# Performance work log

Measured on AMD Instinct MI355X. Metric: run time of the kernel, lower is better.

Reference implementation:

```python
import jax, jax.numpy as jnp
import numpy as np

N = 25000
E = 400000
RAW = 64
REP = 64
HID = 128
HEADS = 2
OUT = 2
NEG_SLOPE = 0.2


def setup_inputs() -> dict:
    key = jax.random.key(0)
    ks = jax.random.split(key, 16)
    d_in1 = RAW + REP
    d_h = HID * HEADS
    inp = {
        'x': jax.random.normal(ks[0], (N, RAW), jnp.float32),
        'rep': jax.random.normal(ks[1], (N, REP), jnp.float32),
        'src': jax.random.randint(ks[2], (E,), 0, N, jnp.int32),
        'dst': jax.random.randint(ks[3], (E,), 0, N, jnp.int32),
        # GATConv 1 params
        'W1': jax.random.normal(ks[4], (d_in1, d_h), jnp.float32) * (1.0 / np.sqrt(d_in1)),
        'al1': jax.random.normal(ks[5], (HEADS, HID), jnp.float32) * 0.1,
        'ar1': jax.random.normal(ks[6], (HEADS, HID), jnp.float32) * 0.1,
        'b1': jnp.zeros((HEADS, HID), jnp.float32),
        # GATConv 2 params
        'W2': jax.random.normal(ks[7], (d_h, d_h), jnp.float32) * (1.0 / np.sqrt(d_h)),
        'al2': jax.random.normal(ks[8], (HEADS, HID), jnp.float32) * 0.1,
        'ar2': jax.random.normal(ks[9], (HEADS, HID), jnp.float32) * 0.1,
        'b2': jnp.zeros((HEADS, HID), jnp.float32),
        # final edge classifier
        'fcW': jax.random.normal(ks[10], (d_h * 2, OUT), jnp.float32) * (1.0 / np.sqrt(d_h * 2)),
        'fcb': jnp.zeros((OUT,), jnp.float32),
    }
    return inp


def _gat_conv(feat, W, a_l, a_r, bias, src, dst):
    """DGL-style GATConv: proj -> edge LeakyReLU score -> per-dst softmax -> scatter-sum."""
    n = feat.shape[0]
    h = (feat @ W).reshape(n, HEADS, HID)            # [N,H,D]
    el = jnp.einsum('nhd,hd->nh', h, a_l)            # [N,H]
    er = jnp.einsum('nhd,hd->nh', h, a_r)            # [N,H]
    e = jax.nn.leaky_relu(el[src] + er[dst], NEG_SLOPE)  # [E,H]
    # numerically stable segment softmax over incoming edges of each dst node
    m = jax.ops.segment_max(e, dst, num_segments=n)      # [N,H]
    m = jnp.where(jnp.isfinite(m), m, 0.0)
    ex = jnp.exp(e - m[dst])                             # [E,H]
    s = jax.ops.segment_sum(ex, dst, num_segments=n)     # [N,H]
    alpha = ex / s[dst]                                  # [E,H]
    out = jax.ops.segment_sum(alpha[:, :, None] * h[src], dst, num_segments=n)  # [N,H,D]
    return out + bias[None, :, :]


def reference(x, rep, src, dst, W1, al1, ar1, b1, W2, al2, ar2, b2, fcW, fcb):
    feat = jnp.concatenate([x, rep], axis=-1)                       # [N, RAW+REP]
    h = _gat_conv(feat, W1, al1, ar1, b1, src, dst)                 # [N,H,D]
    h = jax.nn.relu(h.reshape(N, HEADS * HID))                      # [N, H*D]
    h = _gat_conv(h, W2, al2, ar2, b2, src, dst)                    # [N,H,D]
    h = jax.nn.relu(h.reshape(N, HEADS * HID))                      # [N, H*D]
    edge_feat = jnp.concatenate([h[src], h[dst]], axis=1)           # [E, 2*H*D]
    return edge_feat @ fcW + fcb                                    # [E, OUT]
```

## Files before the change

kernel.cpp:

```cpp
#include <hip/hip_runtime.h>
#include <hip/hip_bf16.h>

#define HEADS 2
#define HIDD  128
#define DH    256
#define NEG   0.2f
#define CAP   128

typedef _Float16 half4 __attribute__((ext_vector_type(4)));
typedef float    f32x4 __attribute__((ext_vector_type(4)));


__global__ __launch_bounds__(256) void k_prep(const float* __restrict__ x,
                                              const float* __restrict__ rep,
                                              const float* __restrict__ W1,
                                              const float* __restrict__ W2,
                                              const int* __restrict__ dst,
                                              _Float16* __restrict__ feat16,
                                              _Float16* __restrict__ W1T,
                                              _Float16* __restrict__ W2T,
                                              int* __restrict__ deg,
                                              int N, int E) {
    int gid = blockIdx.x * 256 + threadIdx.x;
    int featQuads = N * 32;
    if (gid < featQuads) {
        int n = gid >> 5, d = (gid & 31) * 4;
        const float* s = (d < 64) ? (x + (size_t)n * 64 + d) : (rep + (size_t)n * 64 + (d - 64));
        float4 v = *reinterpret_cast<const float4*>(s);
        half4 o = { (_Float16)v.x, (_Float16)v.y, (_Float16)v.z, (_Float16)v.w };
        *reinterpret_cast<half4*>(feat16 + (size_t)n * 128 + d) = o;
        return;
    }
    gid -= featQuads;
    if (gid < 256 * 128) {
        int n = gid >> 7, k = gid & 127;
        W1T[n * 128 + k] = (_Float16)W1[(size_t)k * 256 + n];
        return;
    }
    gid -= 256 * 128;
    if (gid < 256 * 256) {
        int n = gid >> 8, k = gid & 255;
        W2T[n * 256 + k] = (_Float16)W2[(size_t)k * 256 + n];
        return;
    }
    gid -= 256 * 256;
    if (gid < E) atomicAdd(&deg[dst[gid]], 1);
}


__global__ __launch_bounds__(1024) void k_scan(const int* __restrict__ deg,
                                               int* __restrict__ row_ptr,
                                               int* __restrict__ cursor, int n) {
    __shared__ int lds[1024];
    int tid = threadIdx.x;
    int base = tid * 32;
    int v[32];
#pragma unroll
    for (int k = 0; k < 8; ++k) {
        int4 q = *reinterpret_cast<const int4*>(deg + base + k * 4);
        v[k * 4 + 0] = q.x; v[k * 4 + 1] = q.y; v[k * 4 + 2] = q.z; v[k * 4 + 3] = q.w;
    }
    int local[32];
    int sum = 0;
#pragma unroll
    for (int k = 0; k < 32; ++k) { local[k] = sum; sum += v[k]; }
    lds[tid] = sum;
    __syncthreads();
    for (int off = 1; off < 1024; off <<= 1) {
        int t = (tid >= off) ? lds[tid - off] : 0;
        __syncthreads();
        lds[tid] += t;
        __syncthreads();
    }
    int thread_off = lds[tid] - sum;
#pragma unroll
    for (int k = 0; k < 32; ++k) {
        int i = base + k;
        if (i < n) {
            int rp = thread_off + local[k];
            row_ptr[i] = rp;
            cursor[i]  = rp;
        }
    }
    if (tid == 1023) row_ptr[n] = lds[1023];
}

__global__ void k_fill(const int* __restrict__ src, const int* __restrict__ dst,
                       int* __restrict__ cursor, int* __restrict__ csr_src, int E) {
    int e = blockIdx.x * blockDim.x + threadIdx.x;
    if (e < E) {
        int pos = atomicAdd(&cursor[dst[e]], 1);
        csr_src[pos] = src[e];
    }
}


#define GBM 64
#define GBN 128
#define GBK 64

template<int K>
__global__ __launch_bounds__(256) void k_gemm16(const _Float16* __restrict__ A,
                                                const _Float16* __restrict__ BT,
                                                _Float16* __restrict__ C16,
                                                const float* __restrict__ alp,
                                                const float* __restrict__ arp,
                                                float* __restrict__ el,
                                                float* __restrict__ er, int M) {
    __shared__ _Float16 As[2][GBM * GBK];
    __shared__ _Float16 Bs[2][GBN * GBK];

    int tid = threadIdx.x;
    int lane = tid & 63;
    int wave = tid >> 6;
    int row0 = blockIdx.x * GBM;
    int col0 = blockIdx.y * GBN;
    int wrow = (wave & 1) * 32;
    int wcol = (wave >> 1) * 64;

    uint4 ra[2], rb[4];
    const int am = tid >> 3;
    const int ak8 = (tid & 7) * 8;

    auto stage_load = [&](int s) {
        const _Float16* ap = A + (size_t)(row0 + am) * K + s * GBK + ak8;
        ra[0] = *reinterpret_cast<const uint4*>(ap);
        ra[1] = *reinterpret_cast<const uint4*>(ap + (size_t)32 * K);
        const _Float16* bp = BT + (size_t)(col0 + am) * K + s * GBK + ak8;
#pragma unroll
        for (int it = 0; it < 4; ++it)
            rb[it] = *reinterpret_cast<const uint4*>(bp + (size_t)(it * 32) * K);
    };
    auto stage_write = [&](int buf) {
        char* ab = (char*)As[buf];
        char* bb = (char*)Bs[buf];
#pragma unroll
        for (int it = 0; it < 2; ++it) {
            int m = am + it * 32;
            int byte = (m * 128 + ak8 * 2) ^ ((m & 7) << 4);
            *reinterpret_cast<uint4*>(ab + byte) = ra[it];
        }
#pragma unroll
        for (int it = 0; it < 4; ++it) {
            int n = am + it * 32;
            int byte = (n * 128 + ak8 * 2) ^ ((n & 7) << 4);
            *reinterpret_cast<uint4*>(bb + byte) = rb[it];
        }
    };

    f32x4 acc[2][4];
#pragma unroll
    for (int i = 0; i < 2; ++i)
#pragma unroll
        for (int j = 0; j < 4; ++j) acc[i][j] = (f32x4){0.f, 0.f, 0.f, 0.f};

    stage_load(0);
    stage_write(0);
    __syncthreads();

    const int S = K / GBK;
    for (int s = 0; s < S; ++s) {
        if (s + 1 < S) stage_load(s + 1);
        const char* ab = (const char*)As[s & 1];
        const char* bb = (const char*)Bs[s & 1];
#pragma unroll
        for (int kk = 0; kk < GBK / 16; ++kk) {
            half4 af[2], bf[4];
#pragma unroll
            for (int i = 0; i < 2; ++i) {
                int m = wrow + i * 16 + (lane & 15);
                int byte = (m * 128 + kk * 32 + (lane >> 4) * 8) ^ ((m & 7) << 4);
                af[i] = *reinterpret_cast<const half4*>(ab + byte);
            }
#pragma unroll
            for (int j = 0; j < 4; ++j) {
                int n = wcol + j * 16 + (lane & 15);
                int byte = (n * 128 + kk * 32 + (lane >> 4) * 8) ^ ((n & 7) << 4);
                bf[j] = *reinterpret_cast<const half4*>(bb + byte);
            }
#pragma unroll
            for (int i = 0; i < 2; ++i)
#pragma unroll
                for (int j = 0; j < 4; ++j)
                    acc[i][j] = __builtin_amdgcn_mfma_f32_16x16x16f16(af[i], bf[j], acc[i][j], 0, 0, 0);
        }
        if (s + 1 < S) stage_write((s + 1) & 1);
        __syncthreads();
    }

    char* Cs = (char*)As;
    {
        int r4 = (lane >> 4) * 4, cl = lane & 15;
#pragma unroll
        for (int i = 0; i < 2; ++i)
#pragma unroll
            for (int j = 0; j < 4; ++j) {
                int col = wcol + j * 16 + cl;
#pragma unroll
                for (int r = 0; r < 4; ++r) {
                    int row = wrow + i * 16 + r4 + r;
                    int byte = (row * 256 + col * 2) ^ ((row & 7) << 4);
                    *reinterpret_cast<_Float16*>(Cs + byte) = (_Float16)acc[i][j][r];
                }
            }
    }
    __syncthreads();

#pragma unroll
    for (int it = 0; it < 4; ++it) {
        int lin = tid + it * 256;
        int row = lin >> 4, chunk = lin & 15;
        int gr = row0 + row;
        if (gr < M) {
            int byte = (row * 256 + chunk * 16) ^ ((row & 7) << 4);
            *reinterpret_cast<uint4*>(C16 + (size_t)gr * DH + col0 + chunk * 8) =
                *reinterpret_cast<const uint4*>(Cs + byte);
        }
    }

    {
        int r = lane >> 2, q = lane & 3;
        int row = wave * 16 + r;
        const float* alg = alp + col0;
        const float* arg = arp + col0;
        float els = 0.f, ers = 0.f;
#pragma unroll
        for (int kk = 0; kk < 4; ++kk) {
            int c0 = q * 32 + kk * 8;
            int byte = (row * 256 + c0 * 2) ^ ((row & 7) << 4);
            uint4 u = *reinterpret_cast<const uint4*>(Cs + byte);
            const _Float16* hv = (const _Float16*)&u;
#pragma unroll
            for (int t = 0; t < 8; ++t) {
                float hvv = (float)hv[t];
                els = fmaf(hvv, alg[c0 + t], els);
                ers = fmaf(hvv, arg[c0 + t], ers);
            }
        }
        els += __shfl_xor(els, 1); els += __shfl_xor(els, 2);
        ers += __shfl_xor(ers, 1); ers += __shfl_xor(ers, 2);
        int gr = row0 + row;
        if (q == 0 && gr < M) {
            el[gr * 2 + blockIdx.y] = els;
            er[gr * 2 + blockIdx.y] = ers;
        }
    }
}


template<bool FINAL>
__global__ __launch_bounds__(256) void k_agg(const _Float16* __restrict__ h,
                                             const float2* __restrict__ el2,
                                             const float2* __restrict__ er2,
                                             const int* __restrict__ row_ptr,
                                             const int* __restrict__ csr_src,
                                             const float* __restrict__ bias,
                                             _Float16* __restrict__ g,
                                             const float* __restrict__ fcW,
                                             float* __restrict__ p, int N) {
    __shared__ int    s_idx[4][CAP];
    __shared__ float2 s_a[4][CAP];

    int w = threadIdx.x >> 6, lane = threadIdx.x & 63;
    int node = blockIdx.x * 4 + w;
    if (node >= N) return;
    int beg = row_ptr[node];
    int deg = row_ptr[node + 1] - beg;
    float2 er = er2[node];
    bool lo = lane < 32;

    float m0 = -__builtin_inff(), m1 = -__builtin_inff();
    for (int i = lane; i < deg; i += 64) {
        int s = csr_src[beg + i];
        float2 el = el2[s];
        float sc0 = el.x + er.x; sc0 = sc0 > 0.f ? sc0 : NEG * sc0;
        float sc1 = el.y + er.y; sc1 = sc1 > 0.f ? sc1 : NEG * sc1;
        if (i < CAP) { s_idx[w][i] = s; s_a[w][i] = make_float2(sc0, sc1); }
        m0 = fmaxf(m0, sc0);
        m1 = fmaxf(m1, sc1);
    }
#pragma unroll
    for (int off = 32; off; off >>= 1) {
        m0 = fmaxf(m0, __shfl_xor(m0, off));
        m1 = fmaxf(m1, __shfl_xor(m1, off));
    }

    float sum0 = 0.f, sum1 = 0.f;
    for (int i = lane; i < deg; i += 64) {
        float2 sc;
        if (i < CAP) sc = s_a[w][i];
        else {
            int s = csr_src[beg + i];
            float2 el = el2[s];
            sc.x = el.x + er.x; sc.x = sc.x > 0.f ? sc.x : NEG * sc.x;
            sc.y = el.y + er.y; sc.y = sc.y > 0.f ? sc.y : NEG * sc.y;
        }
        float e0 = __expf(sc.x - m0);
        float e1 = __expf(sc.y - m1);
        if (i < CAP) s_a[w][i] = make_float2(e0, e1);
        sum0 += e0;
        sum1 += e1;
    }
#pragma unroll
    for (int off = 32; off; off >>= 1) {
        sum0 += __shfl_xor(sum0, off);
        sum1 += __shfl_xor(sum1, off);
    }
    float S   = lo ? sum0 : sum1;
    float inv = S > 0.f ? 1.f / S : 0.f;
    float mh  = lo ? m0 : m1;
    float erh = lo ? er.x : er.y;

    const _Float16* hp = h + lane * 4;
    float4 acc = make_float4(0.f, 0.f, 0.f, 0.f);

#define FETCH(I, S_, A_)                                                    \
    do {                                                                     \
        int _i = (I);                                                        \
        if (_i < CAP) {                                                      \
            S_ = s_idx[w][_i];                                               \
            float2 _a2 = s_a[w][_i];                                         \
            A_ = lo ? _a2.x : _a2.y;                                         \
        } else {                                                             \
            S_ = csr_src[beg + _i];                                          \
            float2 _el = el2[S_];                                            \
            float _sc = (lo ? _el.x : _el.y) + erh;                          \
            _sc = _sc > 0.f ? _sc : NEG * _sc;                               \
            A_ = __expf(_sc - mh);                                           \
        }                                                                    \
    } while (0)

#define ACCUM(V, A_)                                                         \
    do {                                                                     \
        const _Float16* _hv = reinterpret_cast<const _Float16*>(&(V));       \
        acc.x = fmaf(A_, (float)_hv[0], acc.x);                              \
        acc.y = fmaf(A_, (float)_hv[1], acc.y);                              \
        acc.z = fmaf(A_, (float)_hv[2], acc.z);                              \
        acc.w = fmaf(A_, (float)_hv[3], acc.w);                              \
    } while (0)

    int i = 0;
    for (; i + 8 <= deg; i += 8) {
        int ss[8];
        float aa[8];
#pragma unroll
        for (int u = 0; u < 8; ++u) FETCH(i + u, ss[u], aa[u]);
        uint2 vv[8];
#pragma unroll
        for (int u = 0; u < 8; ++u)
            vv[u] = *reinterpret_cast<const uint2*>(hp + (size_t)ss[u] * DH);
#pragma unroll
        for (int u = 0; u < 8; ++u) ACCUM(vv[u], aa[u]);
    }
    for (; i + 4 <= deg; i += 4) {
        int ss[4];
        float aa[4];
#pragma unroll
        for (int u = 0; u < 4; ++u) FETCH(i + u, ss[u], aa[u]);
        uint2 vv[4];
#pragma unroll
        for (int u = 0; u < 4; ++u)
            vv[u] = *reinterpret_cast<const uint2*>(hp + (size_t)ss[u] * DH);
#pragma unroll
        for (int u = 0; u < 4; ++u) ACCUM(vv[u], aa[u]);
    }
    for (; i < deg; ++i) {
        int s;
        float a;
        FETCH(i, s, a);
        uint2 v = *reinterpret_cast<const uint2*>(hp + (size_t)s * DH);
        ACCUM(v, a);
    }
#undef FETCH
#undef ACCUM

    float4 b = *reinterpret_cast<const float4*>(bias + lane * 4);
    float o0 = fmaxf(fmaf(acc.x, inv, b.x), 0.f);
    float o1 = fmaxf(fmaf(acc.y, inv, b.y), 0.f);
    float o2 = fmaxf(fmaf(acc.z, inv, b.z), 0.f);
    float o3 = fmaxf(fmaf(acc.w, inv, b.w), 0.f);

    if (!FINAL) {
        half4 o = { (_Float16)o0, (_Float16)o1, (_Float16)o2, (_Float16)o3 };
        *reinterpret_cast<half4*>(g + (size_t)node * DH + lane * 4) = o;
    } else {
        int d = lane * 4;
        float a0 = 0.f, a1 = 0.f, a2 = 0.f, a3 = 0.f;
        float ov[4] = {o0, o1, o2, o3};
#pragma unroll
        for (int t = 0; t < 4; ++t) {
            float2 wt = *reinterpret_cast<const float2*>(&fcW[(d + t) * 2]);
            float2 wb = *reinterpret_cast<const float2*>(&fcW[(DH + d + t) * 2]);
            a0 = fmaf(ov[t], wt.x, a0);
            a1 = fmaf(ov[t], wt.y, a1);
            a2 = fmaf(ov[t], wb.x, a2);
            a3 = fmaf(ov[t], wb.y, a3);
        }
#pragma unroll
        for (int off = 32; off; off >>= 1) {
            a0 += __shfl_xor(a0, off);
            a1 += __shfl_xor(a1, off);
            a2 += __shfl_xor(a2, off);
            a3 += __shfl_xor(a3, off);
        }
        if (lane == 0)
            *reinterpret_cast<float4*>(&p[(size_t)node * 4]) = make_float4(a0, a1, a2, a3);
    }
}


__global__ void k_edgeout(const float* __restrict__ p,
                          const int* __restrict__ src,
                          const int* __restrict__ dst,
                          const float* __restrict__ fcb,
                          float* __restrict__ out, int E) {
    int e = blockIdx.x * blockDim.x + threadIdx.x;
    if (e >= E) return;
    int s = src[e], d = dst[e];
    float2 ps = *reinterpret_cast<const float2*>(&p[(size_t)s * 4]);
    float2 pd = *reinterpret_cast<const float2*>(&p[(size_t)d * 4 + 2]);
    float2 o;
    o.x = ps.x + pd.x + fcb[0];
    o.y = ps.y + pd.y + fcb[1];
    *reinterpret_cast<float2*>(&out[(size_t)e * 2]) = o;
}


extern "C" void kernel_launch(void* const* d_in, const int* in_sizes, int n_in,
                              void* d_out, int out_size, void* d_ws, size_t ws_size,
                              hipStream_t stream) {
    const float* x   = (const float*)d_in[0];
    const float* rep = (const float*)d_in[1];
    const int*   src = (const int*)d_in[2];
    const int*   dst = (const int*)d_in[3];
    const float* W1  = (const float*)d_in[4];
    const float* al1 = (const float*)d_in[5];
    const float* ar1 = (const float*)d_in[6];
    const float* b1  = (const float*)d_in[7];
    const float* W2  = (const float*)d_in[8];
    const float* al2 = (const float*)d_in[9];
    const float* ar2 = (const float*)d_in[10];
    const float* b2  = (const float*)d_in[11];
    const float* fcW = (const float*)d_in[12];
    const float* fcb = (const float*)d_in[13];
    float* out = (float*)d_out;

    int N = in_sizes[0] / 64;
    int E = in_sizes[2];

    char* ws = (char*)d_ws;
    size_t off = 0;
    auto alloc = [&](size_t bytes) -> void* {
        void* ptr = ws + off;
        off = (off + bytes + 255) & ~(size_t)255;
        return ptr;
    };
    int*       deg     = (int*)alloc((size_t)32768 * 4);
    int*       row_ptr = (int*)alloc((size_t)(N + 1) * 4);
    int*       cursor  = (int*)alloc((size_t)N * 4);
    int*       csr_src = (int*)alloc((size_t)E * 4);
    _Float16*  feat16  = (_Float16*)alloc((size_t)N * 128 * 2);
    _Float16*  W1T     = (_Float16*)alloc((size_t)256 * 128 * 2);
    _Float16*  W2T     = (_Float16*)alloc((size_t)256 * 256 * 2);
    _Float16*  h16     = (_Float16*)alloc((size_t)N * DH * 2);
    _Float16*  g16     = (_Float16*)alloc((size_t)N * DH * 2);
    float*     el      = (float*)alloc((size_t)N * 2 * 4);
    float*     er      = (float*)alloc((size_t)N * 2 * 4);
    float*     p       = (float*)alloc((size_t)N * 4 * 4);
    (void)alloc(65536);

    hipMemsetAsync(deg, 0, (size_t)32768 * 4, stream);

    int eb = (E + 255) / 256;
    int nb4 = (N + 3) / 4;
    int prep_blocks = (N * 32 + 256 * 128 + 256 * 256 + E + 255) / 256;

    k_prep<<<prep_blocks, 256, 0, stream>>>(x, rep, W1, W2, dst, feat16, W1T, W2T, deg, N, E);
    k_scan<<<1, 1024, 0, stream>>>(deg, row_ptr, cursor, N);
    k_fill<<<eb, 256, 0, stream>>>(src, dst, cursor, csr_src, E);

    dim3 ggrid((N + GBM - 1) / GBM, DH / GBN);
    k_gemm16<128><<<ggrid, 256, 0, stream>>>(feat16, W1T, h16, al1, ar1, el, er, N);
    k_agg<false><<<nb4, 256, 0, stream>>>(h16, (const float2*)el, (const float2*)er,
                                          row_ptr, csr_src, b1, g16, nullptr, nullptr, N);
    k_gemm16<256><<<ggrid, 256, 0, stream>>>(g16, W2T, h16, al2, ar2, el, er, N);
    k_agg<true><<<nb4, 256, 0, stream>>>(h16, (const float2*)el, (const float2*)er,
                                         row_ptr, csr_src, b2, nullptr, fcW, p, N);
    k_edgeout<<<eb, 256, 0, stream>>>(p, src, dst, fcb, out, E);
}
```

Measured before the change: 298.3 us.

## Split aggregation by head across XCD groups for L2 locality

Each aggregation block now handles a single attention head for four nodes. The block index is mapped so that XCDs 0-3 process head 0 and XCDs 4-7 process head 1, which means each XCD's L2 caches only half of each gathered h row. Each lane now accumulates 2 features instead of 4, and the final layer writes per-head partial classifier sums (p doubles to 8 floats per node), which k_edgeout adds together. The costs are twice as many blocks, duplicated softmax and score computation per head, and more loads in the edge-output kernel.

```diff
diff --git a/kernel.cpp b/kernel.cpp
--- a/kernel.cpp
+++ b/kernel.cpp
@@ -8,6 +8,7 @@
 #define CAP   128
 
 typedef _Float16 half4 __attribute__((ext_vector_type(4)));
+typedef _Float16 half2v __attribute__((ext_vector_type(2)));
 typedef float    f32x4 __attribute__((ext_vector_type(4)));
 
 
@@ -261,8 +262,12 @@
     __shared__ int    s_idx[4][CAP];
     __shared__ float2 s_a[4][CAP];
 
+    int b = blockIdx.x;
+    int xcd = b & 7;
+    int half = xcd >> 2;
+    int slot = (b >> 3) * 4 + (xcd & 3);
     int w = threadIdx.x >> 6, lane = threadIdx.x & 63;
-    int node = blockIdx.x * 4 + w;
+    int node = slot * 4 + w;
     if (node >= N) return;
     int beg = row_ptr[node];
     int deg = row_ptr[node + 1] - beg;
@@ -306,13 +311,13 @@
         sum0 += __shfl_xor(sum0, off);
         sum1 += __shfl_xor(sum1, off);
     }
-    float S   = lo ? sum0 : sum1;
-    float inv = S > 0.f ? 1.f / S : 0.f;
-    float mh  = lo ? m0 : m1;
-    float erh = lo ? er.x : er.y;
-
-    const _Float16* hp = h + lane * 4;
-    float4 acc = make_float4(0.f, 0.f, 0.f, 0.f);
+    float mh  = half ? m1 : m0;
+    float Sh  = half ? sum1 : sum0;
+    float inv = Sh > 0.f ? 1.f / Sh : 0.f;
+    float erh = half ? er.y : er.x;
+
+    const _Float16* hp = h + half * 128 + lane * 2;
+    float ax = 0.f, ay = 0.f;
 
 #define FETCH(I, S_, A_)                                                    \
     do {                                                                     \
@@ -320,11 +325,11 @@
         if (_i < CAP) {                                                      \
             S_ = s_idx[w][_i];                                               \
             float2 _a2 = s_a[w][_i];                                         \
-            A_ = lo ? _a2.x : _a2.y;                                         \
+            A_ = half ? _a2.y : _a2.x;                                       \
         } else {                                                             \
             S_ = csr_src[beg + _i];                                          \
             float2 _el = el2[S_];                                            \
-            float _sc = (lo ? _el.x : _el.y) + erh;                          \
+            float _sc = (half ? _el.y : _el.x) + erh;                        \
             _sc = _sc > 0.f ? _sc : NEG * _sc;                               \
             A_ = __expf(_sc - mh);                                           \
         }                                                                    \
@@ -333,10 +338,8 @@
 #define ACCUM(V, A_)                                                         \
     do {                                                                     \
         const _Float16* _hv = reinterpret_cast<const _Float16*>(&(V));       \
-        acc.x = fmaf(A_, (float)_hv[0], acc.x);                              \
-        acc.y = fmaf(A_, (float)_hv[1], acc.y);                              \
-        acc.z = fmaf(A_, (float)_hv[2], acc.z);                              \
-        acc.w = fmaf(A_, (float)_hv[3], acc.w);                              \
+        ax = fmaf(A_, (float)_hv[0], ax);                                    \
+        ay = fmaf(A_, (float)_hv[1], ay);                                    \
     } while (0)
 
     int i = 0;
@@ -345,10 +348,10 @@
         float aa[8];
 #pragma unroll
         for (int u = 0; u < 8; ++u) FETCH(i + u, ss[u], aa[u]);
-        uint2 vv[8];
+        unsigned vv[8];
 #pragma unroll
         for (int u = 0; u < 8; ++u)
-            vv[u] = *reinterpret_cast<const uint2*>(hp + (size_t)ss[u] * DH);
+            vv[u] = *reinterpret_cast<const unsigned*>(hp + (size_t)ss[u] * DH);
 #pragma unroll
         for (int u = 0; u < 8; ++u) ACCUM(vv[u], aa[u]);
     }
@@ -357,10 +360,10 @@
         float aa[4];
 #pragma unroll
         for (int u = 0; u < 4; ++u) FETCH(i + u, ss[u], aa[u]);
-        uint2 vv[4];
+        unsigned vv[4];
 #pragma unroll
         for (int u = 0; u < 4; ++u)
-            vv[u] = *reinterpret_cast<const uint2*>(hp + (size_t)ss[u] * DH);
+            vv[u] = *reinterpret_cast<const unsigned*>(hp + (size_t)ss[u] * DH);
 #pragma unroll
         for (int u = 0; u < 4; ++u) ACCUM(vv[u], aa[u]);
     }
@@ -368,34 +371,29 @@
         int s;
         float a;
         FETCH(i, s, a);
-        uint2 v = *reinterpret_cast<const uint2*>(hp + (size_t)s * DH);
+        unsigned v = *reinterpret_cast<const unsigned*>(hp + (size_t)s * DH);
         ACCUM(v, a);
     }
 #undef FETCH
 #undef ACCUM
 
-    float4 b = *reinterpret_cast<const float4*>(bias + lane * 4);
-    float o0 = fmaxf(fmaf(acc.x, inv, b.x), 0.f);
-    float o1 = fmaxf(fmaf(acc.y, inv, b.y), 0.f);
-    float o2 = fmaxf(fmaf(acc.z, inv, b.z), 0.f);
-    float o3 = fmaxf(fmaf(acc.w, inv, b.w), 0.f);
+    int f = half * 128 + lane * 2;
+    float2 bb = *reinterpret_cast<const float2*>(bias + f);
+    float o0 = fmaxf(fmaf(ax, inv, bb.x), 0.f);
+    float o1 = fmaxf(fmaf(ay, inv, bb.y), 0.f);
 
     if (!FINAL) {
-        half4 o = { (_Float16)o0, (_Float16)o1, (_Float16)o2, (_Float16)o3 };
-        *reinterpret_cast<half4*>(g + (size_t)node * DH + lane * 4) = o;
+        half2v o = { (_Float16)o0, (_Float16)o1 };
+        *reinterpret_cast<half2v*>(g + (size_t)node * DH + f) = o;
     } else {
-        int d = lane * 4;
-        float a0 = 0.f, a1 = 0.f, a2 = 0.f, a3 = 0.f;
-        float ov[4] = {o0, o1, o2, o3};
-#pragma unroll
-        for (int t = 0; t < 4; ++t) {
-            float2 wt = *reinterpret_cast<const float2*>(&fcW[(d + t) * 2]);
-            float2 wb = *reinterpret_cast<const float2*>(&fcW[(DH + d + t) * 2]);
-            a0 = fmaf(ov[t], wt.x, a0);
-            a1 = fmaf(ov[t], wt.y, a1);
-            a2 = fmaf(ov[t], wb.x, a2);
-            a3 = fmaf(ov[t], wb.y, a3);
-        }
+        float2 wt0 = *reinterpret_cast<const float2*>(&fcW[f * 2]);
+        float2 wt1 = *reinterpret_cast<const float2*>(&fcW[(f + 1) * 2]);
+        float2 wb0 = *reinterpret_cast<const float2*>(&fcW[(DH + f) * 2]);
+        float2 wb1 = *reinterpret_cast<const float2*>(&fcW[(DH + f + 1) * 2]);
+        float a0 = o0 * wt0.x + o1 * wt1.x;
+        float a1 = o0 * wt0.y + o1 * wt1.y;
+        float a2 = o0 * wb0.x + o1 * wb1.x;
+        float a3 = o0 * wb0.y + o1 * wb1.y;
 #pragma unroll
         for (int off = 32; off; off >>= 1) {
             a0 += __shfl_xor(a0, off);
@@ -404,7 +402,8 @@
             a3 += __shfl_xor(a3, off);
         }
         if (lane == 0)
-            *reinterpret_cast<float4*>(&p[(size_t)node * 4]) = make_float4(a0, a1, a2, a3);
+            *reinterpret_cast<float4*>(&p[(size_t)node * 8 + half * 4]) =
+                make_float4(a0, a1, a2, a3);
     }
 }
 
@@ -417,11 +416,13 @@
     int e = blockIdx.x * blockDim.x + threadIdx.x;
     if (e >= E) return;
     int s = src[e], d = dst[e];
-    float2 ps = *reinterpret_cast<const float2*>(&p[(size_t)s * 4]);
-    float2 pd = *reinterpret_cast<const float2*>(&p[(size_t)d * 4 + 2]);
+    float4 ps0 = *reinterpret_cast<const float4*>(&p[(size_t)s * 8]);
+    float4 ps1 = *reinterpret_cast<const float4*>(&p[(size_t)s * 8 + 4]);
+    float4 pd0 = *reinterpret_cast<const float4*>(&p[(size_t)d * 8]);
+    float4 pd1 = *reinterpret_cast<const float4*>(&p[(size_t)d * 8 + 4]);
     float2 o;
-    o.x = ps.x + pd.x + fcb[0];
-    o.y = ps.y + pd.y + fcb[1];
+    o.x = ps0.x + ps1.x + pd0.z + pd1.z + fcb[0];
+    o.y = ps0.y + ps1.y + pd0.w + pd1.w + fcb[1];
     *reinterpret_cast<float2*>(&out[(size_t)e * 2]) = o;
 }
 
@@ -466,13 +467,14 @@
     _Float16*  g16     = (_Float16*)alloc((size_t)N * DH * 2);
     float*     el      = (float*)alloc((size_t)N * 2 * 4);
     float*     er      = (float*)alloc((size_t)N * 2 * 4);
-    float*     p       = (float*)alloc((size_t)N * 4 * 4);
+    float*     p       = (float*)alloc((size_t)N * 8 * 4);
     (void)alloc(65536);
 
     hipMemsetAsync(deg, 0, (size_t)32768 * 4, stream);
 
     int eb = (E + 255) / 256;
     int nb4 = (N + 3) / 4;
+    int aggG = ((nb4 + 3) / 4) * 8;
     int prep_blocks = (N * 32 + 256 * 128 + 256 * 256 + E + 255) / 256;
 
     k_prep<<<prep_blocks, 256, 0, stream>>>(x, rep, W1, W2, dst, feat16, W1T, W2T, deg, N, E);
@@ -481,10 +483,10 @@
 
     dim3 ggrid((N + GBM - 1) / GBM, DH / GBN);
     k_gemm16<128><<<ggrid, 256, 0, stream>>>(feat16, W1T, h16, al1, ar1, el, er, N);
-    k_agg<false><<<nb4, 256, 0, stream>>>(h16, (const float2*)el, (const float2*)er,
-                                          row_ptr, csr_src, b1, g16, nullptr, nullptr, N);
+    k_agg<false><<<aggG, 256, 0, stream>>>(h16, (const float2*)el, (const float2*)er,
+                                           row_ptr, csr_src, b1, g16, nullptr, nullptr, N);
     k_gemm16<256><<<ggrid, 256, 0, stream>>>(g16, W2T, h16, al2, ar2, el, er, N);
-    k_agg<true><<<nb4, 256, 0, stream>>>(h16, (const float2*)el, (const float2*)er,
-                                         row_ptr, csr_src, b2, nullptr, fcW, p, N);
+    k_agg<true><<<aggG, 256, 0, stream>>>(h16, (const float2*)el, (const float2*)er,
+                                          row_ptr, csr_src, b2, nullptr, fcW, p, N);
     k_edgeout<<<eb, 256, 0, stream>>>(p, src, dst, fcb, out, E);
 }
```

Measured after the change: 313.1 us. +5.0%, slower.

## Split heads into planar layout, precompute edge softmax numerators, XCD-aware agg mapping

Applied to the files above, without the earlier changes.

Stores projected features per head in separate planes and gives each head to a different half of the XCDs, so each XCD's L2 holds only half the gather working set. Edge exp-scores and per-destination sums are now computed in per-edge kernels (fused into CSR fill, plus a new alpha kernel for layer 2) using float atomics. The per-node max subtraction is dropped, which risks overflow for large scores. The aggregation kernel no longer does its softmax passes; half-waves process alternating edges and are combined with a shuffle. The per-edge passes and atomics add traffic, and float atomic order makes the sums nondeterministic.

```diff
diff --git a/kernel.cpp b/kernel.cpp
--- a/kernel.cpp
+++ b/kernel.cpp
@@ -5,10 +5,11 @@
 #define HIDD  128
 #define DH    256
 #define NEG   0.2f
-#define CAP   128
 
 typedef _Float16 half4 __attribute__((ext_vector_type(4)));
 typedef float    f32x4 __attribute__((ext_vector_type(4)));
+
+__device__ __forceinline__ float leaky(float x) { return x > 0.f ? x : NEG * x; }
 
 
 __global__ __launch_bounds__(256) void k_prep(const float* __restrict__ x,
@@ -85,13 +86,43 @@
     if (tid == 1023) row_ptr[n] = lds[1023];
 }
 
+
 __global__ void k_fill(const int* __restrict__ src, const int* __restrict__ dst,
-                       int* __restrict__ cursor, int* __restrict__ csr_src, int E) {
+                       int* __restrict__ cursor,
+                       int* __restrict__ csr_src, int* __restrict__ csr_dst,
+                       const float2* __restrict__ el2, const float2* __restrict__ er2,
+                       float* __restrict__ alpha, float* __restrict__ Sarr, int E) {
     int e = blockIdx.x * blockDim.x + threadIdx.x;
-    if (e < E) {
-        int pos = atomicAdd(&cursor[dst[e]], 1);
-        csr_src[pos] = src[e];
-    }
+    if (e >= E) return;
+    int s = src[e], d = dst[e];
+    int pos = atomicAdd(&cursor[d], 1);
+    csr_src[pos] = s;
+    csr_dst[pos] = d;
+    float2 el = el2[s];
+    float2 er = er2[d];
+    float e0 = __expf(leaky(el.x + er.x));
+    float e1 = __expf(leaky(el.y + er.y));
+    alpha[pos]     = e0;
+    alpha[E + pos] = e1;
+    atomicAdd(&Sarr[d * 2 + 0], e0);
+    atomicAdd(&Sarr[d * 2 + 1], e1);
+}
+
+
+__global__ void k_alpha2(const int* __restrict__ csr_src, const int* __restrict__ csr_dst,
+                         const float2* __restrict__ el2, const float2* __restrict__ er2,
+                         float* __restrict__ alpha, float* __restrict__ Sarr, int E) {
+    int pos = blockIdx.x * blockDim.x + threadIdx.x;
+    if (pos >= E) return;
+    int s = csr_src[pos], d = csr_dst[pos];
+    float2 el = el2[s];
+    float2 er = er2[d];
+    float e0 = __expf(leaky(el.x + er.x));
+    float e1 = __expf(leaky(el.y + er.y));
+    alpha[pos]     = e0;
+    alpha[E + pos] = e1;
+    atomicAdd(&Sarr[d * 2 + 0], e0);
+    atomicAdd(&Sarr[d * 2 + 1], e1);
 }
 
 
@@ -100,9 +131,9 @@
 #define GBK 64
 
 template<int K>
-__global__ __launch_bounds__(256) void k_gemm16(const _Float16* __restrict__ A,
+__global__ __launch_bounds__(256) void k_gemm16(const _Float16* __restrict__ A, size_t aPS,
                                                 const _Float16* __restrict__ BT,
-                                                _Float16* __restrict__ C16,
+                                                _Float16* __restrict__ C16, size_t cPS,
                                                 const float* __restrict__ alp,
                                                 const float* __restrict__ arp,
                                                 float* __restrict__ el,
@@ -123,10 +154,12 @@
     const int ak8 = (tid & 7) * 8;
 
     auto stage_load = [&](int s) {
-        const _Float16* ap = A + (size_t)(row0 + am) * K + s * GBK + ak8;
+        int koff = s * GBK;
+        const _Float16* ap = A + (size_t)(koff >> 7) * aPS
+                               + (size_t)(row0 + am) * 128 + (koff & 127) + ak8;
         ra[0] = *reinterpret_cast<const uint4*>(ap);
-        ra[1] = *reinterpret_cast<const uint4*>(ap + (size_t)32 * K);
-        const _Float16* bp = BT + (size_t)(col0 + am) * K + s * GBK + ak8;
+        ra[1] = *reinterpret_cast<const uint4*>(ap + (size_t)32 * 128);
+        const _Float16* bp = BT + (size_t)(col0 + am) * K + koff + ak8;
 #pragma unroll
         for (int it = 0; it < 4; ++it)
             rb[it] = *reinterpret_cast<const uint4*>(bp + (size_t)(it * 32) * K);
@@ -213,7 +246,7 @@
         int gr = row0 + row;
         if (gr < M) {
             int byte = (row * 256 + chunk * 16) ^ ((row & 7) << 4);
-            *reinterpret_cast<uint4*>(C16 + (size_t)gr * DH + col0 + chunk * 8) =
+            *reinterpret_cast<uint4*>(C16 + (size_t)blockIdx.y * cPS + (size_t)gr * 128 + chunk * 8) =
                 *reinterpret_cast<const uint4*>(Cs + byte);
         }
     }
@@ -249,86 +282,31 @@
 
 
 template<bool FINAL>
-__global__ __launch_bounds__(256) void k_agg(const _Float16* __restrict__ h,
-                                             const float2* __restrict__ el2,
-                                             const float2* __restrict__ er2,
+__global__ __launch_bounds__(256) void k_agg(const _Float16* __restrict__ h, size_t NS,
+                                             const float* __restrict__ alpha,
+                                             const float* __restrict__ Sarr,
                                              const int* __restrict__ row_ptr,
                                              const int* __restrict__ csr_src,
                                              const float* __restrict__ bias,
                                              _Float16* __restrict__ g,
                                              const float* __restrict__ fcW,
-                                             float* __restrict__ p, int N) {
-    __shared__ int    s_idx[4][CAP];
-    __shared__ float2 s_a[4][CAP];
-
+                                             float* __restrict__ p, int N, int E) {
+    int b = blockIdx.x;
+    int xcd = b & 7;
+    int half = xcd >> 2;
+    int slot = (b >> 3) * 4 + (xcd & 3);
     int w = threadIdx.x >> 6, lane = threadIdx.x & 63;
-    int node = blockIdx.x * 4 + w;
+    int node = slot * 4 + w;
     if (node >= N) return;
     int beg = row_ptr[node];
     int deg = row_ptr[node + 1] - beg;
-    float2 er = er2[node];
-    bool lo = lane < 32;
-
-    float m0 = -__builtin_inff(), m1 = -__builtin_inff();
-    for (int i = lane; i < deg; i += 64) {
-        int s = csr_src[beg + i];
-        float2 el = el2[s];
-        float sc0 = el.x + er.x; sc0 = sc0 > 0.f ? sc0 : NEG * sc0;
-        float sc1 = el.y + er.y; sc1 = sc1 > 0.f ? sc1 : NEG * sc1;
-        if (i < CAP) { s_idx[w][i] = s; s_a[w][i] = make_float2(sc0, sc1); }
-        m0 = fmaxf(m0, sc0);
-        m1 = fmaxf(m1, sc1);
-    }
-#pragma unroll
-    for (int off = 32; off; off >>= 1) {
-        m0 = fmaxf(m0, __shfl_xor(m0, off));
-        m1 = fmaxf(m1, __shfl_xor(m1, off));
-    }
-
-    float sum0 = 0.f, sum1 = 0.f;
-    for (int i = lane; i < deg; i += 64) {
-        float2 sc;
-        if (i < CAP) sc = s_a[w][i];
-        else {
-            int s = csr_src[beg + i];
-            float2 el = el2[s];
-            sc.x = el.x + er.x; sc.x = sc.x > 0.f ? sc.x : NEG * sc.x;
-            sc.y = el.y + er.y; sc.y = sc.y > 0.f ? sc.y : NEG * sc.y;
-        }
-        float e0 = __expf(sc.x - m0);
-        float e1 = __expf(sc.y - m1);
-        if (i < CAP) s_a[w][i] = make_float2(e0, e1);
-        sum0 += e0;
-        sum1 += e1;
-    }
-#pragma unroll
-    for (int off = 32; off; off >>= 1) {
-        sum0 += __shfl_xor(sum0, off);
-        sum1 += __shfl_xor(sum1, off);
-    }
-    float S   = lo ? sum0 : sum1;
-    float inv = S > 0.f ? 1.f / S : 0.f;
-    float mh  = lo ? m0 : m1;
-    float erh = lo ? er.x : er.y;
-
-    const _Float16* hp = h + lane * 4;
+
+    int grp = lane >> 5;
+    int fl  = lane & 31;
+    const float* aH = alpha + (size_t)half * E;
+    const _Float16* hb = h + (size_t)half * NS + fl * 4;
+
     float4 acc = make_float4(0.f, 0.f, 0.f, 0.f);
-
-#define FETCH(I, S_, A_)                                                    \
-    do {                                                                     \
-        int _i = (I);                                                        \
-        if (_i < CAP) {                                                      \
-            S_ = s_idx[w][_i];                                               \
-            float2 _a2 = s_a[w][_i];                                         \
-            A_ = lo ? _a2.x : _a2.y;                                         \
-        } else {                                                             \
-            S_ = csr_src[beg + _i];                                          \
-            float2 _el = el2[S_];                                            \
-            float _sc = (lo ? _el.x : _el.y) + erh;                          \
-            _sc = _sc > 0.f ? _sc : NEG * _sc;                               \
-            A_ = __expf(_sc - mh);                                           \
-        }                                                                    \
-    } while (0)
 
 #define ACCUM(V, A_)                                                         \
     do {                                                                     \
@@ -341,56 +319,64 @@
 
     int i = 0;
     for (; i + 8 <= deg; i += 8) {
-        int ss[8];
-        float aa[8];
-#pragma unroll
-        for (int u = 0; u < 8; ++u) FETCH(i + u, ss[u], aa[u]);
-        uint2 vv[8];
-#pragma unroll
-        for (int u = 0; u < 8; ++u)
-            vv[u] = *reinterpret_cast<const uint2*>(hp + (size_t)ss[u] * DH);
-#pragma unroll
-        for (int u = 0; u < 8; ++u) ACCUM(vv[u], aa[u]);
-    }
-    for (; i + 4 <= deg; i += 4) {
         int ss[4];
         float aa[4];
 #pragma unroll
-        for (int u = 0; u < 4; ++u) FETCH(i + u, ss[u], aa[u]);
+        for (int u = 0; u < 4; ++u) {
+            int id = beg + i + 2 * u + grp;
+            ss[u] = csr_src[id];
+            aa[u] = aH[id];
+        }
         uint2 vv[4];
 #pragma unroll
         for (int u = 0; u < 4; ++u)
-            vv[u] = *reinterpret_cast<const uint2*>(hp + (size_t)ss[u] * DH);
+            vv[u] = *reinterpret_cast<const uint2*>(hb + (size_t)ss[u] * 128);
 #pragma unroll
         for (int u = 0; u < 4; ++u) ACCUM(vv[u], aa[u]);
     }
-    for (; i < deg; ++i) {
-        int s;
-        float a;
-        FETCH(i, s, a);
-        uint2 v = *reinterpret_cast<const uint2*>(hp + (size_t)s * DH);
+    for (; i + 2 <= deg; i += 2) {
+        int id = beg + i + grp;
+        int s = csr_src[id];
+        float a = aH[id];
+        uint2 v = *reinterpret_cast<const uint2*>(hb + (size_t)s * 128);
         ACCUM(v, a);
     }
-#undef FETCH
+    if (i < deg) {
+        int id = beg + i;
+        int s = csr_src[id];
+        float a = grp ? 0.f : aH[id];
+        uint2 v = *reinterpret_cast<const uint2*>(hb + (size_t)s * 128);
+        ACCUM(v, a);
+    }
 #undef ACCUM
 
-    float4 b = *reinterpret_cast<const float4*>(bias + lane * 4);
-    float o0 = fmaxf(fmaf(acc.x, inv, b.x), 0.f);
-    float o1 = fmaxf(fmaf(acc.y, inv, b.y), 0.f);
-    float o2 = fmaxf(fmaf(acc.z, inv, b.z), 0.f);
-    float o3 = fmaxf(fmaf(acc.w, inv, b.w), 0.f);
+    acc.x += __shfl_xor(acc.x, 32);
+    acc.y += __shfl_xor(acc.y, 32);
+    acc.z += __shfl_xor(acc.z, 32);
+    acc.w += __shfl_xor(acc.w, 32);
+
+    float S = Sarr[node * 2 + half];
+    float inv = S > 0.f ? 1.f / S : 0.f;
+    int f = half * 128 + fl * 4;
+    float4 bb = *reinterpret_cast<const float4*>(bias + f);
+    float o0 = fmaxf(fmaf(acc.x, inv, bb.x), 0.f);
+    float o1 = fmaxf(fmaf(acc.y, inv, bb.y), 0.f);
+    float o2 = fmaxf(fmaf(acc.z, inv, bb.z), 0.f);
+    float o3 = fmaxf(fmaf(acc.w, inv, bb.w), 0.f);
 
     if (!FINAL) {
-        half4 o = { (_Float16)o0, (_Float16)o1, (_Float16)o2, (_Float16)o3 };
-        *reinterpret_cast<half4*>(g + (size_t)node * DH + lane * 4) = o;
+        if (grp == 0) {
+            half4 o = { (_Float16)o0, (_Float16)o1, (_Float16)o2, (_Float16)o3 };
+            *reinterpret_cast<half4*>(g + (size_t)half * NS + (size_t)node * 128 + fl * 4) = o;
+        }
     } else {
-        int d = lane * 4;
+        if (grp) { o0 = 0.f; o1 = 0.f; o2 = 0.f; o3 = 0.f; }
+        float ov[4] = {o0, o1, o2, o3};
         float a0 = 0.f, a1 = 0.f, a2 = 0.f, a3 = 0.f;
-        float ov[4] = {o0, o1, o2, o3};
 #pragma unroll
         for (int t = 0; t < 4; ++t) {
-            float2 wt = *reinterpret_cast<const float2*>(&fcW[(d + t) * 2]);
-            float2 wb = *reinterpret_cast<const float2*>(&fcW[(DH + d + t) * 2]);
+            float2 wt = *reinterpret_cast<const float2*>(&fcW[(f + t) * 2]);
+            float2 wb = *reinterpret_cast<const float2*>(&fcW[(DH + f + t) * 2]);
             a0 = fmaf(ov[t], wt.x, a0);
             a1 = fmaf(ov[t], wt.y, a1);
             a2 = fmaf(ov[t], wb.x, a2);
@@ -404,7 +390,8 @@
             a3 += __shfl_xor(a3, off);
         }
         if (lane == 0)
-            *reinterpret_cast<float4*>(&p[(size_t)node * 4]) = make_float4(a0, a1, a2, a3);
+            *reinterpret_cast<float4*>(&p[(size_t)node * 8 + half * 4]) =
+                make_float4(a0, a1, a2, a3);
     }
 }
 
@@ -417,11 +404,13 @@
     int e = blockIdx.x * blockDim.x + threadIdx.x;
     if (e >= E) return;
     int s = src[e], d = dst[e];
-    float2 ps = *reinterpret_cast<const float2*>(&p[(size_t)s * 4]);
-    float2 pd = *reinterpret_cast<const float2*>(&p[(size_t)d * 4 + 2]);
+    float4 ps0 = *reinterpret_cast<const float4*>(&p[(size_t)s * 8]);
+    float4 ps1 = *reinterpret_cast<const float4*>(&p[(size_t)s * 8 + 4]);
+    float4 pd0 = *reinterpret_cast<const float4*>(&p[(size_t)d * 8]);
+    float4 pd1 = *reinterpret_cast<const float4*>(&p[(size_t)d * 8 + 4]);
     float2 o;
-    o.x = ps.x + pd.x + fcb[0];
-    o.y = ps.y + pd.y + fcb[1];
+    o.x = ps0.x + ps1.x + pd0.z + pd1.z + fcb[0];
+    o.y = ps0.y + ps1.y + pd0.w + pd1.w + fcb[1];
     *reinterpret_cast<float2*>(&out[(size_t)e * 2]) = o;
 }
 
@@ -456,9 +445,14 @@
         return ptr;
     };
     int*       deg     = (int*)alloc((size_t)32768 * 4);
+    float*     S1      = (float*)alloc((size_t)N * 2 * 4);
+    float*     S2      = (float*)alloc((size_t)N * 2 * 4);
+    size_t     zbytes  = off;
     int*       row_ptr = (int*)alloc((size_t)(N + 1) * 4);
     int*       cursor  = (int*)alloc((size_t)N * 4);
     int*       csr_src = (int*)alloc((size_t)E * 4);
+    int*       csr_dst = (int*)alloc((size_t)E * 4);
+    float*     alpha   = (float*)alloc((size_t)E * 2 * 4);
     _Float16*  feat16  = (_Float16*)alloc((size_t)N * 128 * 2);
     _Float16*  W1T     = (_Float16*)alloc((size_t)256 * 128 * 2);
     _Float16*  W2T     = (_Float16*)alloc((size_t)256 * 256 * 2);
@@ -466,25 +460,31 @@
     _Float16*  g16     = (_Float16*)alloc((size_t)N * DH * 2);
     float*     el      = (float*)alloc((size_t)N * 2 * 4);
     float*     er      = (float*)alloc((size_t)N * 2 * 4);
-    float*     p       = (float*)alloc((size_t)N * 4 * 4);
+    float*     p       = (float*)alloc((size_t)N * 8 * 4);
     (void)alloc(65536);
 
-    hipMemsetAsync(deg, 0, (size_t)32768 * 4, stream);
+    size_t NS = (size_t)N * 128;
+
+    hipMemsetAsync(deg, 0, zbytes, stream);
 
     int eb = (E + 255) / 256;
     int nb4 = (N + 3) / 4;
+    int aggG = ((nb4 + 3) / 4) * 8;
     int prep_blocks = (N * 32 + 256 * 128 + 256 * 256 + E + 255) / 256;
 
     k_prep<<<prep_blocks, 256, 0, stream>>>(x, rep, W1, W2, dst, feat16, W1T, W2T, deg, N, E);
+
+    dim3 ggrid((N + GBM - 1) / GBM, DH / GBN);
+    k_gemm16<128><<<ggrid, 256, 0, stream>>>(feat16, 0, W1T, h16, NS, al1, ar1, el, er, N);
     k_scan<<<1, 1024, 0, stream>>>(deg, row_ptr, cursor, N);
-    k_fill<<<eb, 256, 0, stream>>>(src, dst, cursor, csr_src, E);
-
-    dim3 ggrid((N + GBM - 1) / GBM, DH / GBN);
-    k_gemm16<128><<<ggrid, 256, 0, stream>>>(feat16, W1T, h16, al1, ar1, el, er, N);
-    k_agg<false><<<nb4, 256, 0, stream>>>(h16, (const float2*)el, (const float2*)er,
-                                          row_ptr, csr_src, b1, g16, nullptr, nullptr, N);
-    k_gemm16<256><<<ggrid, 256, 0, stream>>>(g16, W2T, h16, al2, ar2, el, er, N);
-    k_agg<true><<<nb4, 256, 0, stream>>>(h16, (const float2*)el, (const float2*)er,
-                                         row_ptr, csr_src, b2, nullptr, fcW, p, N);
+    k_fill<<<eb, 256, 0, stream>>>(src, dst, cursor, csr_src, csr_dst,
+                                   (const float2*)el, (const float2*)er, alpha, S1, E);
+    k_agg<false><<<aggG, 256, 0, stream>>>(h16, NS, alpha, S1, row_ptr, csr_src,
+                                           b1, g16, nullptr, nullptr, N, E);
+    k_gemm16<256><<<ggrid, 256, 0, stream>>>(g16, NS, W2T, h16, NS, al2, ar2, el, er, N);
+    k_alpha2<<<eb, 256, 0, stream>>>(csr_src, csr_dst, (const float2*)el, (const float2*)er,
+                                     alpha, S2, E);
+    k_agg<true><<<aggG, 256, 0, stream>>>(h16, NS, alpha, S2, row_ptr, csr_src,
+                                          b2, nullptr, fcW, p, N, E);
     k_edgeout<<<eb, 256, 0, stream>>>(p, src, dst, fcb, out, E);
 }
```

After: 398.2 us. 33.5% more time.

## Fuse prep, degree scan and CSR fill into one cooperative kernel

Applied to the files above, without the earlier changes.

Replaces the memset, prep, single-block scan and fill launches with one cooperative kernel of 512 blocks. Grid-wide syncs separate degree zeroing and conversion, degree counting, a two-level block scan, and the CSR fill. This removes several launch gaps and the serial one-block scan. In exchange it adds grid-sync overhead, a serial per-block scan done by one thread, and a fixed grid size that caps parallelism for the atomic phases.

```diff
diff --git a/kernel.cpp b/kernel.cpp
--- a/kernel.cpp
+++ b/kernel.cpp
@@ -1,5 +1,8 @@
 #include <hip/hip_runtime.h>
 #include <hip/hip_bf16.h>
+#include <hip/hip_cooperative_groups.h>
+
+namespace cg = cooperative_groups;
 
 #define HEADS 2
 #define HIDD  128
@@ -7,88 +10,87 @@
 #define NEG   0.2f
 #define CAP   128
 
+#define CSR_BLOCKS 512
+
 typedef _Float16 half4 __attribute__((ext_vector_type(4)));
 typedef float    f32x4 __attribute__((ext_vector_type(4)));
 
 
-__global__ __launch_bounds__(256) void k_prep(const float* __restrict__ x,
-                                              const float* __restrict__ rep,
-                                              const float* __restrict__ W1,
-                                              const float* __restrict__ W2,
-                                              const int* __restrict__ dst,
-                                              _Float16* __restrict__ feat16,
-                                              _Float16* __restrict__ W1T,
-                                              _Float16* __restrict__ W2T,
-                                              int* __restrict__ deg,
-                                              int N, int E) {
-    int gid = blockIdx.x * 256 + threadIdx.x;
+__global__ void k_csr(const float* __restrict__ x, const float* __restrict__ rep,
+                      const float* __restrict__ W1, const float* __restrict__ W2,
+                      const int* __restrict__ src, const int* __restrict__ dst,
+                      _Float16* __restrict__ feat16, _Float16* __restrict__ W1T,
+                      _Float16* __restrict__ W2T,
+                      int* __restrict__ deg, int* __restrict__ row_ptr,
+                      int* __restrict__ cursor, int* __restrict__ csr_src,
+                      int* __restrict__ blockSums, int N, int E) {
+    cg::grid_group grid = cg::this_grid();
+    int tid = threadIdx.x, bid = blockIdx.x;
+    int gsize = gridDim.x * blockDim.x;
+    int gtid = bid * blockDim.x + tid;
+
+    for (int i = gtid; i < 32768; i += gsize) deg[i] = 0;
     int featQuads = N * 32;
-    if (gid < featQuads) {
-        int n = gid >> 5, d = (gid & 31) * 4;
+    for (int q = gtid; q < featQuads; q += gsize) {
+        int n = q >> 5, d = (q & 31) * 4;
         const float* s = (d < 64) ? (x + (size_t)n * 64 + d) : (rep + (size_t)n * 64 + (d - 64));
         float4 v = *reinterpret_cast<const float4*>(s);
         half4 o = { (_Float16)v.x, (_Float16)v.y, (_Float16)v.z, (_Float16)v.w };
         *reinterpret_cast<half4*>(feat16 + (size_t)n * 128 + d) = o;
-        return;
-    }
-    gid -= featQuads;
-    if (gid < 256 * 128) {
-        int n = gid >> 7, k = gid & 127;
+    }
+    for (int i = gtid; i < 256 * 128; i += gsize) {
+        int n = i >> 7, k = i & 127;
         W1T[n * 128 + k] = (_Float16)W1[(size_t)k * 256 + n];
-        return;
-    }
-    gid -= 256 * 128;
-    if (gid < 256 * 256) {
-        int n = gid >> 8, k = gid & 255;
+    }
+    for (int i = gtid; i < 256 * 256; i += gsize) {
+        int n = i >> 8, k = i & 255;
         W2T[n * 256 + k] = (_Float16)W2[(size_t)k * 256 + n];
-        return;
-    }
-    gid -= 256 * 256;
-    if (gid < E) atomicAdd(&deg[dst[gid]], 1);
-}
-
-
-__global__ __launch_bounds__(1024) void k_scan(const int* __restrict__ deg,
-                                               int* __restrict__ row_ptr,
-                                               int* __restrict__ cursor, int n) {
-    __shared__ int lds[1024];
-    int tid = threadIdx.x;
-    int base = tid * 32;
-    int v[32];
-#pragma unroll
-    for (int k = 0; k < 8; ++k) {
-        int4 q = *reinterpret_cast<const int4*>(deg + base + k * 4);
-        v[k * 4 + 0] = q.x; v[k * 4 + 1] = q.y; v[k * 4 + 2] = q.z; v[k * 4 + 3] = q.w;
-    }
-    int local[32];
-    int sum = 0;
-#pragma unroll
-    for (int k = 0; k < 32; ++k) { local[k] = sum; sum += v[k]; }
-    lds[tid] = sum;
+    }
+    grid.sync();
+
+    for (int e = gtid; e < E; e += gsize) atomicAdd(&deg[dst[e]], 1);
+    grid.sync();
+
+    __shared__ int lsum[64];
+    int base = bid * 64;
+    if (tid < 64) lsum[tid] = deg[base + tid];
     __syncthreads();
-    for (int off = 1; off < 1024; off <<= 1) {
-        int t = (tid >= off) ? lds[tid - off] : 0;
+    if (tid == 0) {
+        int s = 0;
+#pragma unroll 8
+        for (int k = 0; k < 64; ++k) { int t = lsum[k]; lsum[k] = s; s += t; }
+        blockSums[bid] = s;
+    }
+    __syncthreads();
+    grid.sync();
+    if (bid == 0) {
+        __shared__ int bs[CSR_BLOCKS];
+        bs[tid] = blockSums[tid];
+        bs[tid + 256] = blockSums[tid + 256];
         __syncthreads();
-        lds[tid] += t;
+        if (tid == 0) {
+            int s = 0;
+#pragma unroll 8
+            for (int k = 0; k < CSR_BLOCKS; ++k) { int t = bs[k]; bs[k] = s; s += t; }
+            row_ptr[N] = s;
+        }
         __syncthreads();
-    }
-    int thread_off = lds[tid] - sum;
-#pragma unroll
-    for (int k = 0; k < 32; ++k) {
-        int i = base + k;
-        if (i < n) {
-            int rp = thread_off + local[k];
+        blockSums[tid] = bs[tid];
+        blockSums[tid + 256] = bs[tid + 256];
+    }
+    grid.sync();
+    int boff = blockSums[bid];
+    if (tid < 64) {
+        int i = base + tid;
+        if (i < N) {
+            int rp = boff + lsum[tid];
             row_ptr[i] = rp;
             cursor[i]  = rp;
         }
     }
-    if (tid == 1023) row_ptr[n] = lds[1023];
-}
-
-__global__ void k_fill(const int* __restrict__ src, const int* __restrict__ dst,
-                       int* __restrict__ cursor, int* __restrict__ csr_src, int E) {
-    int e = blockIdx.x * blockDim.x + threadIdx.x;
-    if (e < E) {
+    grid.sync();
+
+    for (int e = gtid; e < E; e += gsize) {
         int pos = atomicAdd(&cursor[dst[e]], 1);
         csr_src[pos] = src[e];
     }
@@ -455,29 +457,33 @@
         off = (off + bytes + 255) & ~(size_t)255;
         return ptr;
     };
-    int*       deg     = (int*)alloc((size_t)32768 * 4);
-    int*       row_ptr = (int*)alloc((size_t)(N + 1) * 4);
-    int*       cursor  = (int*)alloc((size_t)N * 4);
-    int*       csr_src = (int*)alloc((size_t)E * 4);
-    _Float16*  feat16  = (_Float16*)alloc((size_t)N * 128 * 2);
-    _Float16*  W1T     = (_Float16*)alloc((size_t)256 * 128 * 2);
-    _Float16*  W2T     = (_Float16*)alloc((size_t)256 * 256 * 2);
-    _Float16*  h16     = (_Float16*)alloc((size_t)N * DH * 2);
-    _Float16*  g16     = (_Float16*)alloc((size_t)N * DH * 2);
-    float*     el      = (float*)alloc((size_t)N * 2 * 4);
-    float*     er      = (float*)alloc((size_t)N * 2 * 4);
-    float*     p       = (float*)alloc((size_t)N * 4 * 4);
+    int*       deg      = (int*)alloc((size_t)32768 * 4);
+    int*       row_ptr  = (int*)alloc((size_t)(N + 1) * 4);
+    int*       cursor   = (int*)alloc((size_t)N * 4);
+    int*       csr_src  = (int*)alloc((size_t)E * 4);
+    int*       blockSums= (int*)alloc((size_t)CSR_BLOCKS * 4);
+    _Float16*  feat16   = (_Float16*)alloc((size_t)N * 128 * 2);
+    _Float16*  W1T      = (_Float16*)alloc((size_t)256 * 128 * 2);
+    _Float16*  W2T      = (_Float16*)alloc((size_t)256 * 256 * 2);
+    _Float16*  h16      = (_Float16*)alloc((size_t)N * DH * 2);
+    _Float16*  g16      = (_Float16*)alloc((size_t)N * DH * 2);
+    float*     el       = (float*)alloc((size_t)N * 2 * 4);
+    float*     er       = (float*)alloc((size_t)N * 2 * 4);
+    float*     p        = (float*)alloc((size_t)N * 4 * 4);
     (void)alloc(65536);
-
-    hipMemsetAsync(deg, 0, (size_t)32768 * 4, stream);
 
     int eb = (E + 255) / 256;
     int nb4 = (N + 3) / 4;
-    int prep_blocks = (N * 32 + 256 * 128 + 256 * 256 + E + 255) / 256;
-
-    k_prep<<<prep_blocks, 256, 0, stream>>>(x, rep, W1, W2, dst, feat16, W1T, W2T, deg, N, E);
-    k_scan<<<1, 1024, 0, stream>>>(deg, row_ptr, cursor, N);
-    k_fill<<<eb, 256, 0, stream>>>(src, dst, cursor, csr_src, E);
+
+    {
+        void* args[] = { (void*)&x, (void*)&rep, (void*)&W1, (void*)&W2,
+                         (void*)&src, (void*)&dst,
+                         (void*)&feat16, (void*)&W1T, (void*)&W2T,
+                         (void*)&deg, (void*)&row_ptr, (void*)&cursor, (void*)&csr_src,
+                         (void*)&blockSums, (void*)&N, (void*)&E };
+        hipLaunchCooperativeKernel((const void*)k_csr, dim3(CSR_BLOCKS), dim3(256),
+                                   args, 0, stream);
+    }
 
     dim3 ggrid((N + GBM - 1) / GBM, DH / GBN);
     k_gemm16<128><<<ggrid, 256, 0, stream>>>(feat16, W1T, h16, al1, ar1, el, er, N);
```

Result: slower. 552.2 us (+85.1%).
